# Kernel optimization log

Hardware: AMD Instinct MI355X
Metric: run time of the kernel (lower is better)

## Reference

```python
import jax, jax.numpy as jnp
import numpy as np

N = 100000   # nodes
E = 1600000  # edges (before self-loops)
IN, HID, OUT = 128, 16, 10
NEG_SLOPE = 0.2
LN_EPS = 1e-5


def layer_norm(x, gamma, beta):
    mu = jnp.mean(x, axis=-1, keepdims=True)
    var = jnp.mean((x - mu) ** 2, axis=-1, keepdims=True)
    return (x - mu) * jax.lax.rsqrt(var + LN_EPS) * gamma + beta


def gat_conv(x, edge_index, W, a_src, a_dst, bias, concat):
    # x: [N, Din], W: [Din, H*F], a_src/a_dst: [H, F]
    n = x.shape[0]
    H, F = a_src.shape
    h = (x @ W).reshape(n, H, F)                      # [N, H, F]
    src, dst = edge_index[0], edge_index[1]
    alpha_src = jnp.sum(h * a_src, axis=-1)           # [N, H]
    alpha_dst = jnp.sum(h * a_dst, axis=-1)           # [N, H]
    e = jax.nn.leaky_relu(alpha_src[src] + alpha_dst[dst], NEG_SLOPE)  # [E, H]
    # segment softmax over incoming edges of each dst node (self-loops guarantee non-empty)
    m = jax.ops.segment_max(e, dst, num_segments=n)
    e = jnp.exp(e - m[dst])
    s = jax.ops.segment_sum(e, dst, num_segments=n)
    alpha = e / (s[dst] + 1e-16)                      # [E, H]
    out = jax.ops.segment_sum(h[src] * alpha[:, :, None], dst, num_segments=n)  # [N, H, F]
    out = out.reshape(n, H * F) if concat else out.mean(axis=1)
    return out + bias


def setup_inputs() -> dict:
    key = jax.random.key(0)
    ks = jax.random.split(key, 20)
    d = {}
    d["x"] = jax.random.normal(ks[0], (N, IN), dtype=jnp.float32)
    d["edge_index"] = jax.random.randint(ks[1], (2, E), 0, N, dtype=jnp.int64)
    s = 0.1
    # layer 1: IN -> HID, 8 heads, concat
    d["W1"] = jax.random.normal(ks[2], (IN, 8 * HID), jnp.float32) * s
    d["a_src1"] = jax.random.normal(ks[3], (8, HID), jnp.float32) * s
    d["a_dst1"] = jax.random.normal(ks[4], (8, HID), jnp.float32) * s
    d["b1"] = jnp.zeros((8 * HID,), jnp.float32)
    d["g1"] = jnp.ones((8 * HID,), jnp.float32)
    d["be1"] = jnp.zeros((8 * HID,), jnp.float32)
    # layer 2: 8*HID -> HID, 4 heads, concat
    d["W2"] = jax.random.normal(ks[5], (8 * HID, 4 * HID), jnp.float32) * s
    d["a_src2"] = jax.random.normal(ks[6], (4, HID), jnp.float32) * s
    d["a_dst2"] = jax.random.normal(ks[7], (4, HID), jnp.float32) * s
    d["b2"] = jnp.zeros((4 * HID,), jnp.float32)
    d["g2"] = jnp.ones((4 * HID,), jnp.float32)
    d["be2"] = jnp.zeros((4 * HID,), jnp.float32)
    # layer 3: 4*HID -> OUT, 1 head, no concat
    d["W3"] = jax.random.normal(ks[8], (4 * HID, OUT), jnp.float32) * s
    d["a_src3"] = jax.random.normal(ks[9], (1, OUT), jnp.float32) * s
    d["a_dst3"] = jax.random.normal(ks[10], (1, OUT), jnp.float32) * s
    d["b3"] = jnp.zeros((OUT,), jnp.float32)
    return d


def reference(x, edge_index, W1, a_src1, a_dst1, b1, g1, be1,
              W2, a_src2, a_dst2, b2, g2, be2,
              W3, a_src3, a_dst3, b3):
    n = x.shape[0]
    loops = jnp.arange(n, dtype=edge_index.dtype)
    ei = jnp.concatenate([edge_index, jnp.stack([loops, loops])], axis=1)  # add self-loops
    h = gat_conv(x, ei, W1, a_src1, a_dst1, b1, concat=True)
    h = jax.nn.elu(layer_norm(h, g1, be1))
    h = gat_conv(h, ei, W2, a_src2, a_dst2, b2, concat=True)
    h = jax.nn.elu(layer_norm(h, g2, be2))
    h = gat_conv(h, ei, W3, a_src3, a_dst3, b3, concat=False)
    return jax.nn.log_softmax(h, axis=1)
```

## Files before the change

### kernel.cpp

```cpp
#include <hip/hip_runtime.h>
#include <hip/hip_bf16.h>
#include <math.h>

typedef __hip_bfloat16 bf16;
typedef __bf16 bf16x8 __attribute__((ext_vector_type(8)));
typedef float floatx4 __attribute__((ext_vector_type(4)));

#define CSR_CH  4096
#define CSR_REG 8192

__device__ __forceinline__ unsigned short f2bu(float f) {
    bf16 b = __float2bfloat16(f);
    return __builtin_bit_cast(unsigned short, b);
}
__device__ __forceinline__ float bu2f(unsigned short u) {
    return __uint_as_float(((unsigned)u) << 16);
}

template<int PF>
__device__ __forceinline__ void ldbfv(const unsigned short* p, float* v) {
    if constexpr (PF == 8) {
        uint4 u = *reinterpret_cast<const uint4*>(p);
        v[0] = __uint_as_float(u.x << 16); v[1] = __uint_as_float(u.x & 0xffff0000u);
        v[2] = __uint_as_float(u.y << 16); v[3] = __uint_as_float(u.y & 0xffff0000u);
        v[4] = __uint_as_float(u.z << 16); v[5] = __uint_as_float(u.z & 0xffff0000u);
        v[6] = __uint_as_float(u.w << 16); v[7] = __uint_as_float(u.w & 0xffff0000u);
    } else if constexpr (PF == 4) {
        uint2 u = *reinterpret_cast<const uint2*>(p);
        v[0] = __uint_as_float(u.x << 16); v[1] = __uint_as_float(u.x & 0xffff0000u);
        v[2] = __uint_as_float(u.y << 16); v[3] = __uint_as_float(u.y & 0xffff0000u);
    } else {
        unsigned u = *reinterpret_cast<const unsigned*>(p);
        v[0] = __uint_as_float(u << 16); v[1] = __uint_as_float(u & 0xffff0000u);
    }
}

template<typename XT, int H>
__global__ __launch_bounds__(256) void gemm_mfma(
    const XT* __restrict__ X, const float* __restrict__ W,
    const float* __restrict__ a_src, const float* __restrict__ a_dst,
    bf16* __restrict__ Hout, float* __restrict__ asrc, float* __restrict__ adst,
    int N, int NG, const int* __restrict__ ei, int E, int DPB,
    int* __restrict__ histM)
{
    constexpr int M = H * 16;
    constexpr int KP = 136;
    constexpr int NT = M / 16;
    constexpr int HPQ = H / 4;
    __shared__ __align__(16) unsigned short Wt[M * KP];
    __shared__ __align__(16) unsigned short As[64 * KP];
    __shared__ float As_s[M], Ad_s[M];
    int tid = threadIdx.x;

    if (blockIdx.x >= NG) {
        int* cnt = (int*)Wt;
        cnt[tid] = 0;
        __syncthreads();
        int blk = blockIdx.x - NG;
        int e0 = blk * CSR_CH;
        int e1 = min(E, e0 + CSR_CH);
        for (int e = e0 + tid; e < e1; e += 256)
            atomicAdd(&cnt[ei[E + e] / DPB], 1);
        __syncthreads();
        histM[blk * 256 + tid] = cnt[tid];
        return;
    }

    int r0 = blockIdx.x * 64;
    for (int i = tid; i < M; i += 256) { As_s[i] = a_src[i]; Ad_s[i] = a_dst[i]; }
    for (int idx = tid; idx < 128 * M; idx += 256) {
        int k = idx / M, m = idx % M;
        Wt[m * KP + k] = f2bu(W[idx]);
    }
    if constexpr (__is_same(XT, float)) {
        for (int idx = tid; idx < 64 * 32; idx += 256) {
            int row = idx >> 5, c4 = (idx & 31) * 4;
            int grow = r0 + row;
            float4 v = make_float4(0.f, 0.f, 0.f, 0.f);
            if (grow < N)
                v = *reinterpret_cast<const float4*>(X + (size_t)grow * 128 + c4);
            unsigned short* a = &As[row * KP + c4];
            a[0] = f2bu(v.x); a[1] = f2bu(v.y); a[2] = f2bu(v.z); a[3] = f2bu(v.w);
        }
    } else {
        for (int idx = tid; idx < 64 * 16; idx += 256) {
            int row = idx >> 4, c8 = (idx & 15) * 8;
            int grow = r0 + row;
            uint4 v = make_uint4(0u, 0u, 0u, 0u);
            if (grow < N)
                v = *reinterpret_cast<const uint4*>((const unsigned short*)X + (size_t)grow * 128 + c8);
            *reinterpret_cast<uint4*>(&As[row * KP + c8]) = v;
        }
    }
    __syncthreads();

    int w = tid >> 6, l = tid & 63, q = l >> 4, c = l & 15;
    floatx4 acc[NT];
    #pragma unroll
    for (int t = 0; t < NT; ++t) acc[t] = (floatx4){0.f, 0.f, 0.f, 0.f};

    #pragma unroll
    for (int kc = 0; kc < 4; ++kc) {
        bf16x8 a = *reinterpret_cast<const bf16x8*>(&As[(w * 16 + c) * KP + kc * 32 + q * 8]);
        #pragma unroll
        for (int t = 0; t < NT; ++t) {
            bf16x8 b = *reinterpret_cast<const bf16x8*>(&Wt[(t * 16 + c) * KP + kc * 32 + q * 8]);
            acc[t] = __builtin_amdgcn_mfma_f32_16x16x32_bf16(a, b, acc[t], 0, 0, 0);
        }
    }
    __syncthreads();
    #pragma unroll
    for (int t = 0; t < NT; ++t)
        #pragma unroll
        for (int r = 0; r < 4; ++r)
            As[(w * 16 + q * 4 + r) * KP + t * 16 + c] = f2bu(acc[t][r]);
    __syncthreads();
    for (int idx = tid; idx < 64 * (M / 8); idx += 256) {
        int row = idx / (M / 8), g = idx % (M / 8);
        int grow = r0 + row;
        if (grow < N)
            *reinterpret_cast<uint4*>(Hout + (size_t)grow * M + g * 8) =
                *reinterpret_cast<const uint4*>(&As[row * KP + g * 8]);
    }
    {
        int r = tid >> 2, qq = tid & 3;
        int grow = r0 + r;
        if (grow < N) {
            #pragma unroll
            for (int hh = 0; hh < HPQ; ++hh) {
                int hd = qq * HPQ + hh;
                float s1 = 0.f, s2 = 0.f;
                #pragma unroll
                for (int f = 0; f < 16; f += 2) {
                    unsigned u = *reinterpret_cast<const unsigned*>(&As[r * KP + hd * 16 + f]);
                    float v0 = __uint_as_float(u << 16);
                    float v1 = __uint_as_float(u & 0xffff0000u);
                    s1 += v0 * As_s[hd * 16 + f] + v1 * As_s[hd * 16 + f + 1];
                    s2 += v0 * Ad_s[hd * 16 + f] + v1 * Ad_s[hd * 16 + f + 1];
                }
                asrc[(size_t)grow * H + hd] = s1;
                adst[(size_t)grow * H + hd] = s2;
            }
        }
    }
}

__global__ __launch_bounds__(256) void csr_colscan(
    const int* __restrict__ histM, int NBLK,
    int* __restrict__ offT, int* __restrict__ btot)
{
    __shared__ int sm[512];
    int b = blockIdx.x;
    int tid = threadIdx.x;
    int i0 = tid, i1 = tid + 256;
    sm[i0] = (i0 < NBLK) ? histM[i0 * 256 + b] : 0;
    sm[i1] = (i1 < NBLK) ? histM[i1 * 256 + b] : 0;
    __syncthreads();
    #pragma unroll
    for (int o = 1; o < 512; o <<= 1) {
        int t0 = (i0 >= o) ? sm[i0 - o] : 0;
        int t1 = (i1 >= o) ? sm[i1 - o] : 0;
        __syncthreads();
        sm[i0] += t0; sm[i1] += t1;
        __syncthreads();
    }
    if (i0 < NBLK) offT[b * NBLK + i0] = b * CSR_REG + ((i0 == 0) ? 0 : sm[i0 - 1]);
    if (i1 < NBLK) offT[b * NBLK + i1] = b * CSR_REG + sm[i1 - 1];
    if (tid == 0) btot[b] = sm[511];
}

__global__ __launch_bounds__(256) void csr_pair_scatter(
    const int* __restrict__ ei, int E, int DPB,
    const int* __restrict__ offT, int NBLK,
    unsigned* __restrict__ pairs)
{
    __shared__ int cnt[256];
    int tid = threadIdx.x;
    int blk = blockIdx.x;
    cnt[tid] = offT[tid * NBLK + blk];
    __syncthreads();
    int e0 = blk * CSR_CH;
    int e1 = min(E, e0 + CSR_CH);
    for (int e = e0 + tid; e < e1; e += 256) {
        int s = ei[e];
        int d = ei[E + e];
        int b = d / DPB;
        int dloc = d - b * DPB;
        int pos = atomicAdd(&cnt[b], 1);
        pairs[pos] = ((unsigned)dloc << 17) | (unsigned)s;
    }
}

__global__ __launch_bounds__(256) void csr_fine(
    const unsigned* __restrict__ pairs, const int* __restrict__ btot,
    int DPB, int N, int2* __restrict__ ptrSE, int* __restrict__ col)
{
    __shared__ int sm[512];
    __shared__ int off[512];
    int b = blockIdx.x;
    int tid = threadIdx.x;
    int base = b * CSR_REG;
    int tot = btot[b];
    int d0 = b * DPB;
    int i0 = tid, i1 = tid + 256;
    sm[i0] = 0; sm[i1] = 0;
    __syncthreads();
    for (int i = tid; i < tot; i += 256)
        atomicAdd(&sm[pairs[base + i] >> 17], 1);
    __syncthreads();
    #pragma unroll
    for (int o = 1; o < 512; o <<= 1) {
        int t0 = (i0 >= o) ? sm[i0 - o] : 0;
        int t1 = (i1 >= o) ? sm[i1 - o] : 0;
        __syncthreads();
        sm[i0] += t0; sm[i1] += t1;
        __syncthreads();
    }
    int s0e = base + ((i0 == 0) ? 0 : sm[i0 - 1]);
    int s1e = base + sm[i1 - 1];
    off[i0] = s0e;
    off[i1] = s1e;
    if (i0 < DPB && d0 + i0 < N) ptrSE[d0 + i0] = make_int2(s0e, base + sm[i0]);
    if (i1 < DPB && d0 + i1 < N) ptrSE[d0 + i1] = make_int2(s1e, base + sm[i1]);
    __syncthreads();
    for (int i = tid; i < tot; i += 256) {
        unsigned p = pairs[base + i];
        int pos = atomicAdd(&off[p >> 17], 1);
        col[pos] = (int)(p & 0x1FFFFu);
    }
}

template<int M, int LPD>
__global__ __launch_bounds__(256) void agg_ln_kernel(
    const int2* __restrict__ ptrSE, const int* __restrict__ col,
    const float* __restrict__ asrc, const float* __restrict__ adst,
    const bf16* __restrict__ hb, const float* __restrict__ bias,
    const float* __restrict__ g, const float* __restrict__ be,
    bf16* __restrict__ out, int N)
{
    constexpr int PF = M / LPD;
    constexpr int H = M / 16;
    constexpr int DPBk = 256 / LPD;
    int tid = threadIdx.x;
    int sub = tid / LPD;
    int j = tid % LPD;
    int d = blockIdx.x * DPBk + sub;
    if (d >= N) return;
    int f0 = j * PF;
    int hd = f0 / 16;
    int2 se = ptrSE[d];
    int e = se.x, end = se.y;
    float adst_h = adst[d * H + hd];
    const unsigned short* hw = (const unsigned short*)hb;

    float ac0[PF], ac1[PF];
    float dn0, dn1 = 0.f;
    {
        float lg = asrc[d * H + hd] + adst_h;
        lg = lg > 0.f ? lg : 0.2f * lg;
        float w = __expf(lg);
        float v[PF];
        ldbfv<PF>(hw + (size_t)d * M + f0, v);
        #pragma unroll
        for (int p = 0; p < PF; ++p) { ac0[p] = w * v[p]; ac1[p] = 0.f; }
        dn0 = w;
    }
    for (; e + 4 <= end; e += 4) {
        int s0 = col[e], s1 = col[e + 1], s2 = col[e + 2], s3 = col[e + 3];
        float l0 = asrc[s0 * H + hd];
        float l1 = asrc[s1 * H + hd];
        float l2 = asrc[s2 * H + hd];
        float l3 = asrc[s3 * H + hd];
        float v0[PF], v1[PF], v2[PF], v3[PF];
        ldbfv<PF>(hw + (size_t)s0 * M + f0, v0);
        ldbfv<PF>(hw + (size_t)s1 * M + f0, v1);
        ldbfv<PF>(hw + (size_t)s2 * M + f0, v2);
        ldbfv<PF>(hw + (size_t)s3 * M + f0, v3);
        l0 += adst_h; l0 = l0 > 0.f ? l0 : 0.2f * l0; float w0 = __expf(l0);
        l1 += adst_h; l1 = l1 > 0.f ? l1 : 0.2f * l1; float w1 = __expf(l1);
        l2 += adst_h; l2 = l2 > 0.f ? l2 : 0.2f * l2; float w2 = __expf(l2);
        l3 += adst_h; l3 = l3 > 0.f ? l3 : 0.2f * l3; float w3 = __expf(l3);
        #pragma unroll
        for (int p = 0; p < PF; ++p) {
            ac0[p] += w0 * v0[p];
            ac1[p] += w1 * v1[p];
            ac0[p] += w2 * v2[p];
            ac1[p] += w3 * v3[p];
        }
        dn0 += w0 + w2; dn1 += w1 + w3;
    }
    for (; e < end; ++e) {
        int s = col[e];
        float lg = asrc[s * H + hd] + adst_h;
        lg = lg > 0.f ? lg : 0.2f * lg;
        float w = __expf(lg);
        float v[PF];
        ldbfv<PF>(hw + (size_t)s * M + f0, v);
        #pragma unroll
        for (int p = 0; p < PF; ++p) ac0[p] += w * v[p];
        dn0 += w;
    }

    float rden = 1.f / (dn0 + dn1 + 1e-16f);
    float o[PF];
    float sm1 = 0.f, sm2 = 0.f;
    #pragma unroll
    for (int p = 0; p < PF; ++p) {
        o[p] = (ac0[p] + ac1[p]) * rden + bias[f0 + p];
        sm1 += o[p];
        sm2 += o[p] * o[p];
    }
    #pragma unroll
    for (int off = LPD / 2; off >= 1; off >>= 1) {
        sm1 += __shfl_xor(sm1, off, LPD);
        sm2 += __shfl_xor(sm2, off, LPD);
    }
    float mu = sm1 * (1.f / M);
    float var = sm2 * (1.f / M) - mu * mu;
    float inv = rsqrtf(var + 1e-5f);
    unsigned pk[PF / 2];
    #pragma unroll
    for (int p = 0; p < PF; p += 2) {
        float y0 = (o[p] - mu) * inv * g[f0 + p] + be[f0 + p];
        float y1 = (o[p + 1] - mu) * inv * g[f0 + p + 1] + be[f0 + p + 1];
        y0 = y0 > 0.f ? y0 : expm1f(y0);
        y1 = y1 > 0.f ? y1 : expm1f(y1);
        pk[p / 2] = (unsigned)f2bu(y0) | ((unsigned)f2bu(y1) << 16);
    }
    unsigned short* op = (unsigned short*)out + (size_t)d * M + f0;
    if constexpr (PF == 8)
        *reinterpret_cast<uint4*>(op) = make_uint4(pk[0], pk[1], pk[2], pk[3]);
    else if constexpr (PF == 4)
        *reinterpret_cast<uint2*>(op) = make_uint2(pk[0], pk[1]);
    else
        *reinterpret_cast<unsigned*>(op) = pk[0];
}

__global__ __launch_bounds__(256) void agg_ln_l2_g3(
    const int2* __restrict__ ptrSE, const int* __restrict__ col,
    const float* __restrict__ asrc, const float* __restrict__ adst,
    const bf16* __restrict__ hb, const float* __restrict__ bias,
    const float* __restrict__ g, const float* __restrict__ be,
    const float* __restrict__ W3, const float* __restrict__ as3,
    const float* __restrict__ ad3,
    bf16* __restrict__ h3, float* __restrict__ asrc3, float* __restrict__ adst3,
    int N)
{
    constexpr int M = 64, LPD = 16, PF = 4, H = 4, DPBk = 16;
    __shared__ float Wl[640], s3[10], d3[10];
    int tid = threadIdx.x;
    for (int i = tid; i < 640; i += 256) Wl[i] = W3[i];
    if (tid < 10) { s3[tid] = as3[tid]; d3[tid] = ad3[tid]; }
    __syncthreads();
    int sub = tid >> 4;
    int j = tid & 15;
    int d = blockIdx.x * DPBk + sub;
    if (d >= N) return;
    int f0 = j * PF;
    int hd = f0 / 16;
    int2 se = ptrSE[d];
    int e = se.x, end = se.y;
    float adst_h = adst[d * H + hd];
    const unsigned short* hw = (const unsigned short*)hb;

    float ac0[PF], ac1[PF];
    float dn0, dn1 = 0.f;
    {
        float lg = asrc[d * H + hd] + adst_h;
        lg = lg > 0.f ? lg : 0.2f * lg;
        float w = __expf(lg);
        float v[PF];
        ldbfv<PF>(hw + (size_t)d * M + f0, v);
        #pragma unroll
        for (int p = 0; p < PF; ++p) { ac0[p] = w * v[p]; ac1[p] = 0.f; }
        dn0 = w;
    }
    for (; e + 4 <= end; e += 4) {
        int s0 = col[e], s1 = col[e + 1], s2 = col[e + 2], s3i = col[e + 3];
        float l0 = asrc[s0 * H + hd];
        float l1 = asrc[s1 * H + hd];
        float l2 = asrc[s2 * H + hd];
        float l3 = asrc[s3i * H + hd];
        float v0[PF], v1[PF], v2[PF], v3[PF];
        ldbfv<PF>(hw + (size_t)s0 * M + f0, v0);
        ldbfv<PF>(hw + (size_t)s1 * M + f0, v1);
        ldbfv<PF>(hw + (size_t)s2 * M + f0, v2);
        ldbfv<PF>(hw + (size_t)s3i * M + f0, v3);
        l0 += adst_h; l0 = l0 > 0.f ? l0 : 0.2f * l0; float w0 = __expf(l0);
        l1 += adst_h; l1 = l1 > 0.f ? l1 : 0.2f * l1; float w1 = __expf(l1);
        l2 += adst_h; l2 = l2 > 0.f ? l2 : 0.2f * l2; float w2 = __expf(l2);
        l3 += adst_h; l3 = l3 > 0.f ? l3 : 0.2f * l3; float w3 = __expf(l3);
        #pragma unroll
        for (int p = 0; p < PF; ++p) {
            ac0[p] += w0 * v0[p];
            ac1[p] += w1 * v1[p];
            ac0[p] += w2 * v2[p];
            ac1[p] += w3 * v3[p];
        }
        dn0 += w0 + w2; dn1 += w1 + w3;
    }
    for (; e < end; ++e) {
        int s = col[e];
        float lg = asrc[s * H + hd] + adst_h;
        lg = lg > 0.f ? lg : 0.2f * lg;
        float w = __expf(lg);
        float v[PF];
        ldbfv<PF>(hw + (size_t)s * M + f0, v);
        #pragma unroll
        for (int p = 0; p < PF; ++p) ac0[p] += w * v[p];
        dn0 += w;
    }

    float rden = 1.f / (dn0 + dn1 + 1e-16f);
    float o[PF];
    float sm1 = 0.f, sm2 = 0.f;
    #pragma unroll
    for (int p = 0; p < PF; ++p) {
        o[p] = (ac0[p] + ac1[p]) * rden + bias[f0 + p];
        sm1 += o[p];
        sm2 += o[p] * o[p];
    }
    #pragma unroll
    for (int off = 8; off >= 1; off >>= 1) {
        sm1 += __shfl_xor(sm1, off, 16);
        sm2 += __shfl_xor(sm2, off, 16);
    }
    float mu = sm1 * (1.f / M);
    float var = sm2 * (1.f / M) - mu * mu;
    float inv = rsqrtf(var + 1e-5f);
    float y[PF];
    #pragma unroll
    for (int p = 0; p < PF; ++p) {
        float t = (o[p] - mu) * inv * g[f0 + p] + be[f0 + p];
        y[p] = t > 0.f ? t : expm1f(t);
    }
    float pj[10];
    #pragma unroll
    for (int jj = 0; jj < 10; ++jj)
        pj[jj] = y[0] * Wl[(f0 + 0) * 10 + jj] + y[1] * Wl[(f0 + 1) * 10 + jj]
               + y[2] * Wl[(f0 + 2) * 10 + jj] + y[3] * Wl[(f0 + 3) * 10 + jj];
    #pragma unroll
    for (int off = 8; off >= 1; off >>= 1)
        #pragma unroll
        for (int jj = 0; jj < 10; ++jj)
            pj[jj] += __shfl_xor(pj[jj], off, 16);
    if (j == 0) {
        unsigned short* hr = (unsigned short*)h3 + (size_t)d * 16;
        #pragma unroll
        for (int jj = 0; jj < 10; jj += 2) {
            unsigned u = (unsigned)f2bu(pj[jj]) | ((unsigned)f2bu(pj[jj + 1]) << 16);
            *reinterpret_cast<unsigned*>(hr + jj) = u;
        }
        float a1 = 0.f, a2 = 0.f;
        #pragma unroll
        for (int jj = 0; jj < 10; ++jj) {
            a1 += pj[jj] * s3[jj];
            a2 += pj[jj] * d3[jj];
        }
        asrc3[d] = a1;
        adst3[d] = a2;
    }
}

__global__ __launch_bounds__(256) void agg_l3_final(
    const int2* __restrict__ ptrSE, const int* __restrict__ col,
    const float* __restrict__ asrc, const float* __restrict__ adst,
    const bf16* __restrict__ h, const float* __restrict__ b3,
    float* __restrict__ out, int N)
{
    int tid = threadIdx.x;
    int sub16 = tid >> 4;
    int j = tid & 15;
    int d = blockIdx.x * 16 + sub16;
    if (d >= N) return;
    const unsigned short* hu = (const unsigned short*)h;
    int2 se = ptrSE[d];
    int e = se.x, end = se.y;
    float adst_d = adst[d];
    float lg = asrc[d] + adst_d;
    lg = lg > 0.f ? lg : 0.2f * lg;
    float w = __expf(lg);
    bool act = j < 10;
    float a0 = act ? w * bu2f(hu[(size_t)d * 16 + j]) : 0.f;
    float a1 = 0.f, a2 = 0.f, a3 = 0.f;
    float d0 = w, d1 = 0.f, d2 = 0.f, d3 = 0.f;
    for (; e + 4 <= end; e += 4) {
        int s0 = col[e + 0], s1 = col[e + 1], s2 = col[e + 2], s3 = col[e + 3];
        float l0 = asrc[s0], l1 = asrc[s1], l2 = asrc[s2], l3 = asrc[s3];
        float v0 = act ? bu2f(hu[(size_t)s0 * 16 + j]) : 0.f;
        float v1 = act ? bu2f(hu[(size_t)s1 * 16 + j]) : 0.f;
        float v2 = act ? bu2f(hu[(size_t)s2 * 16 + j]) : 0.f;
        float v3 = act ? bu2f(hu[(size_t)s3 * 16 + j]) : 0.f;
        l0 += adst_d; l0 = l0 > 0.f ? l0 : 0.2f * l0; float w0 = __expf(l0);
        l1 += adst_d; l1 = l1 > 0.f ? l1 : 0.2f * l1; float w1 = __expf(l1);
        l2 += adst_d; l2 = l2 > 0.f ? l2 : 0.2f * l2; float w2 = __expf(l2);
        l3 += adst_d; l3 = l3 > 0.f ? l3 : 0.2f * l3; float w3 = __expf(l3);
        a0 += w0 * v0; a1 += w1 * v1; a2 += w2 * v2; a3 += w3 * v3;
        d0 += w0; d1 += w1; d2 += w2; d3 += w3;
    }
    for (; e < end; ++e) {
        int s = col[e];
        float l = asrc[s] + adst_d;
        l = l > 0.f ? l : 0.2f * l;
        float ww = __expf(l);
        if (act) a0 += ww * bu2f(hu[(size_t)s * 16 + j]);
        d0 += ww;
    }
    float den = d0 + d1 + d2 + d3;
    float v = (a0 + a1 + a2 + a3) / (den + 1e-16f);
    float lv = act ? v + b3[j] : -1e30f;
    float mx = lv;
    #pragma unroll
    for (int off = 1; off < 16; off <<= 1) mx = fmaxf(mx, __shfl_xor(mx, off, 16));
    float ev = act ? __expf(lv - mx) : 0.f;
    float se2 = ev;
    #pragma unroll
    for (int off = 1; off < 16; off <<= 1) se2 += __shfl_xor(se2, off, 16);
    float ls = mx + logf(se2);
    if (act) out[(size_t)d * 10 + j] = lv - ls;
}

static inline int cdiv(long a, long b) { return (int)((a + b - 1) / b); }

extern "C" void kernel_launch(void* const* d_in, const int* in_sizes, int n_in,
                              void* d_out, int out_size, void* d_ws, size_t ws_size,
                              hipStream_t stream)
{
    const float* x   = (const float*)d_in[0];
    const int*   ei  = (const int*)d_in[1];
    const float* W1  = (const float*)d_in[2];
    const float* as1 = (const float*)d_in[3];
    const float* ad1 = (const float*)d_in[4];
    const float* b1  = (const float*)d_in[5];
    const float* g1  = (const float*)d_in[6];
    const float* be1 = (const float*)d_in[7];
    const float* W2  = (const float*)d_in[8];
    const float* as2 = (const float*)d_in[9];
    const float* ad2 = (const float*)d_in[10];
    const float* b2  = (const float*)d_in[11];
    const float* g2  = (const float*)d_in[12];
    const float* be2 = (const float*)d_in[13];
    const float* W3  = (const float*)d_in[14];
    const float* as3 = (const float*)d_in[15];
    const float* ad3 = (const float*)d_in[16];
    const float* b3  = (const float*)d_in[17];

    const int N = in_sizes[0] / 128;
    const int E = in_sizes[1] / 2;

    const int DPB  = cdiv(N, 256);
    const int NBLK = cdiv(E, CSR_CH);

    bf16*     hb    = (bf16*)d_ws;
    bf16*     aggb  = hb + (size_t)N * 128;
    float*    asrc  = (float*)(aggb + (size_t)N * 128);
    float*    adst  = asrc + (size_t)N * 8;
    float*    asrc3 = adst + (size_t)N * 8;
    float*    adst3 = asrc3 + N;
    unsigned* pairs = (unsigned*)(adst3 + N);
    int*      col   = (int*)(pairs + 256 * CSR_REG);
    int2*     ptrSE = (int2*)(col + 256 * CSR_REG);
    int*      histM = (int*)(ptrSE + N);
    int*      offT  = histM + (size_t)NBLK * 256;
    int*      btot  = offT + (size_t)NBLK * 256;
    bf16*     h3b   = aggb;

    const int NG1 = cdiv(N, 64);

    gemm_mfma<float, 8><<<NG1 + NBLK, 256, 0, stream>>>(
        x, W1, as1, ad1, hb, asrc, adst, N, NG1, ei, E, DPB, histM);
    csr_colscan<<<256, 256, 0, stream>>>(histM, NBLK, offT, btot);
    csr_pair_scatter<<<NBLK, 256, 0, stream>>>(ei, E, DPB, offT, NBLK, pairs);
    csr_fine<<<256, 256, 0, stream>>>(pairs, btot, DPB, N, ptrSE, col);

    agg_ln_kernel<128, 16><<<cdiv(N, 16), 256, 0, stream>>>(
        ptrSE, col, asrc, adst, hb, b1, g1, be1, aggb, N);

    const int NG2 = cdiv(N, 64);
    gemm_mfma<bf16, 4><<<NG2, 256, 0, stream>>>(
        aggb, W2, as2, ad2, hb, asrc, adst, N, NG2, nullptr, 0, 1, nullptr);

    agg_ln_l2_g3<<<cdiv(N, 16), 256, 0, stream>>>(
        ptrSE, col, asrc, adst, hb, b2, g2, be2, W3, as3, ad3,
        h3b, asrc3, adst3, N);

    agg_l3_final<<<cdiv(N, 16), 256, 0, stream>>>(
        ptrSE, col, asrc3, adst3, h3b, b3, (float*)d_out, N);
}
```

Measured before the change: 382.6 us.

## Use fewer lanes per node with wider loads and prefetched neighbor indices in aggregation

The three aggregation kernels now assign fewer lanes to each destination node: 8 lanes for layers 1 and 2, and 4 for layer 3. Each lane loads 16-byte vectors of bf16 features and covers more features, so a block handles 32 or 64 nodes instead of 16. The neighbor indices for the next group of four edges are loaded one iteration ahead to hide the latency of the col loads. The aim is fewer, wider gather transactions and less redundant per-lane work such as attention-logit loads and exps, at the cost of more registers per thread and less parallelism per node on high-degree nodes.

```diff
diff --git a/kernel.cpp b/kernel.cpp
--- a/kernel.cpp
+++ b/kernel.cpp
@@ -17,22 +17,21 @@
     return __uint_as_float(((unsigned)u) << 16);
 }
 
-template<int PF>
-__device__ __forceinline__ void ldbfv(const unsigned short* p, float* v) {
-    if constexpr (PF == 8) {
-        uint4 u = *reinterpret_cast<const uint4*>(p);
-        v[0] = __uint_as_float(u.x << 16); v[1] = __uint_as_float(u.x & 0xffff0000u);
-        v[2] = __uint_as_float(u.y << 16); v[3] = __uint_as_float(u.y & 0xffff0000u);
-        v[4] = __uint_as_float(u.z << 16); v[5] = __uint_as_float(u.z & 0xffff0000u);
-        v[6] = __uint_as_float(u.w << 16); v[7] = __uint_as_float(u.w & 0xffff0000u);
-    } else if constexpr (PF == 4) {
-        uint2 u = *reinterpret_cast<const uint2*>(p);
-        v[0] = __uint_as_float(u.x << 16); v[1] = __uint_as_float(u.x & 0xffff0000u);
-        v[2] = __uint_as_float(u.y << 16); v[3] = __uint_as_float(u.y & 0xffff0000u);
-    } else {
-        unsigned u = *reinterpret_cast<const unsigned*>(p);
-        v[0] = __uint_as_float(u << 16); v[1] = __uint_as_float(u & 0xffff0000u);
-    }
+__device__ __forceinline__ void accu4(float* ac, float w, uint4 u) {
+    ac[0] += w * __uint_as_float(u.x << 16);
+    ac[1] += w * __uint_as_float(u.x & 0xffff0000u);
+    ac[2] += w * __uint_as_float(u.y << 16);
+    ac[3] += w * __uint_as_float(u.y & 0xffff0000u);
+    ac[4] += w * __uint_as_float(u.z << 16);
+    ac[5] += w * __uint_as_float(u.z & 0xffff0000u);
+    ac[6] += w * __uint_as_float(u.w << 16);
+    ac[7] += w * __uint_as_float(u.w & 0xffff0000u);
+}
+__device__ __forceinline__ void accu2(float* ac, float w, uint2 u) {
+    ac[0] += w * __uint_as_float(u.x << 16);
+    ac[1] += w * __uint_as_float(u.x & 0xffff0000u);
+    ac[2] += w * __uint_as_float(u.y << 16);
+    ac[3] += w * __uint_as_float(u.y & 0xffff0000u);
 }
 
 template<typename XT, int H>
@@ -230,110 +229,111 @@
     }
 }
 
-template<int M, int LPD>
-__global__ __launch_bounds__(256) void agg_ln_kernel(
+__global__ __launch_bounds__(256) void agg_ln_l1(
     const int2* __restrict__ ptrSE, const int* __restrict__ col,
     const float* __restrict__ asrc, const float* __restrict__ adst,
     const bf16* __restrict__ hb, const float* __restrict__ bias,
     const float* __restrict__ g, const float* __restrict__ be,
     bf16* __restrict__ out, int N)
 {
-    constexpr int PF = M / LPD;
-    constexpr int H = M / 16;
-    constexpr int DPBk = 256 / LPD;
     int tid = threadIdx.x;
-    int sub = tid / LPD;
-    int j = tid % LPD;
-    int d = blockIdx.x * DPBk + sub;
+    int sub = tid >> 3, j = tid & 7;
+    int d = blockIdx.x * 32 + sub;
     if (d >= N) return;
-    int f0 = j * PF;
-    int hd = f0 / 16;
+    int f0 = j * 16;
+    int hd = j;
     int2 se = ptrSE[d];
     int e = se.x, end = se.y;
-    float adst_h = adst[d * H + hd];
+    float adst_h = adst[d * 8 + hd];
     const unsigned short* hw = (const unsigned short*)hb;
-
-    float ac0[PF], ac1[PF];
+    const unsigned short* hwl = hw + f0;
+    const float* as_h = asrc + hd;
+
+    float ac[16];
+    #pragma unroll
+    for (int p = 0; p < 16; ++p) ac[p] = 0.f;
     float dn0, dn1 = 0.f;
+
     {
-        float lg = asrc[d * H + hd] + adst_h;
+        float lg = as_h[(size_t)d * 8] + adst_h;
         lg = lg > 0.f ? lg : 0.2f * lg;
         float w = __expf(lg);
-        float v[PF];
-        ldbfv<PF>(hw + (size_t)d * M + f0, v);
-        #pragma unroll
-        for (int p = 0; p < PF; ++p) { ac0[p] = w * v[p]; ac1[p] = 0.f; }
+        const uint4* p = reinterpret_cast<const uint4*>(hwl + ((size_t)d << 7));
+        uint4 a = p[0], b = p[1];
+        accu4(ac, w, a); accu4(ac + 8, w, b);
         dn0 = w;
     }
-    for (; e + 4 <= end; e += 4) {
-        int s0 = col[e], s1 = col[e + 1], s2 = col[e + 2], s3 = col[e + 3];
-        float l0 = asrc[s0 * H + hd];
-        float l1 = asrc[s1 * H + hd];
-        float l2 = asrc[s2 * H + hd];
-        float l3 = asrc[s3 * H + hd];
-        float v0[PF], v1[PF], v2[PF], v3[PF];
-        ldbfv<PF>(hw + (size_t)s0 * M + f0, v0);
-        ldbfv<PF>(hw + (size_t)s1 * M + f0, v1);
-        ldbfv<PF>(hw + (size_t)s2 * M + f0, v2);
-        ldbfv<PF>(hw + (size_t)s3 * M + f0, v3);
+
+    int c0 = 0, c1 = 0, c2 = 0, c3 = 0;
+    if (e + 4 <= end) { c0 = col[e]; c1 = col[e + 1]; c2 = col[e + 2]; c3 = col[e + 3]; }
+    while (e + 4 <= end) {
+        int en = e + 4;
+        int n0 = c0, n1 = c1, n2 = c2, n3 = c3;
+        if (en + 4 <= end) { n0 = col[en]; n1 = col[en + 1]; n2 = col[en + 2]; n3 = col[en + 3]; }
+        float l0 = as_h[(size_t)c0 * 8];
+        float l1 = as_h[(size_t)c1 * 8];
+        float l2 = as_h[(size_t)c2 * 8];
+        float l3 = as_h[(size_t)c3 * 8];
+        const uint4* p0 = reinterpret_cast<const uint4*>(hwl + ((size_t)c0 << 7));
+        const uint4* p1 = reinterpret_cast<const uint4*>(hwl + ((size_t)c1 << 7));
+        const uint4* p2 = reinterpret_cast<const uint4*>(hwl + ((size_t)c2 << 7));
+        const uint4* p3 = reinterpret_cast<const uint4*>(hwl + ((size_t)c3 << 7));
+        uint4 u00 = p0[0], u01 = p0[1];
+        uint4 u10 = p1[0], u11 = p1[1];
+        uint4 u20 = p2[0], u21 = p2[1];
+        uint4 u30 = p3[0], u31 = p3[1];
         l0 += adst_h; l0 = l0 > 0.f ? l0 : 0.2f * l0; float w0 = __expf(l0);
         l1 += adst_h; l1 = l1 > 0.f ? l1 : 0.2f * l1; float w1 = __expf(l1);
         l2 += adst_h; l2 = l2 > 0.f ? l2 : 0.2f * l2; float w2 = __expf(l2);
         l3 += adst_h; l3 = l3 > 0.f ? l3 : 0.2f * l3; float w3 = __expf(l3);
-        #pragma unroll
-        for (int p = 0; p < PF; ++p) {
-            ac0[p] += w0 * v0[p];
-            ac1[p] += w1 * v1[p];
-            ac0[p] += w2 * v2[p];
-            ac1[p] += w3 * v3[p];
-        }
+        accu4(ac, w0, u00); accu4(ac + 8, w0, u01);
+        accu4(ac, w1, u10); accu4(ac + 8, w1, u11);
+        accu4(ac, w2, u20); accu4(ac + 8, w2, u21);
+        accu4(ac, w3, u30); accu4(ac + 8, w3, u31);
         dn0 += w0 + w2; dn1 += w1 + w3;
+        c0 = n0; c1 = n1; c2 = n2; c3 = n3;
+        e = en;
     }
     for (; e < end; ++e) {
         int s = col[e];
-        float lg = asrc[s * H + hd] + adst_h;
+        float lg = as_h[(size_t)s * 8] + adst_h;
         lg = lg > 0.f ? lg : 0.2f * lg;
         float w = __expf(lg);
-        float v[PF];
-        ldbfv<PF>(hw + (size_t)s * M + f0, v);
-        #pragma unroll
-        for (int p = 0; p < PF; ++p) ac0[p] += w * v[p];
+        const uint4* p = reinterpret_cast<const uint4*>(hwl + ((size_t)s << 7));
+        uint4 a = p[0], b = p[1];
+        accu4(ac, w, a); accu4(ac + 8, w, b);
         dn0 += w;
     }
 
     float rden = 1.f / (dn0 + dn1 + 1e-16f);
-    float o[PF];
+    float o[16];
     float sm1 = 0.f, sm2 = 0.f;
     #pragma unroll
-    for (int p = 0; p < PF; ++p) {
-        o[p] = (ac0[p] + ac1[p]) * rden + bias[f0 + p];
+    for (int p = 0; p < 16; ++p) {
+        o[p] = ac[p] * rden + bias[f0 + p];
         sm1 += o[p];
         sm2 += o[p] * o[p];
     }
     #pragma unroll
-    for (int off = LPD / 2; off >= 1; off >>= 1) {
-        sm1 += __shfl_xor(sm1, off, LPD);
-        sm2 += __shfl_xor(sm2, off, LPD);
-    }
-    float mu = sm1 * (1.f / M);
-    float var = sm2 * (1.f / M) - mu * mu;
+    for (int off = 4; off >= 1; off >>= 1) {
+        sm1 += __shfl_xor(sm1, off, 8);
+        sm2 += __shfl_xor(sm2, off, 8);
+    }
+    float mu = sm1 * (1.f / 128.f);
+    float var = sm2 * (1.f / 128.f) - mu * mu;
     float inv = rsqrtf(var + 1e-5f);
-    unsigned pk[PF / 2];
-    #pragma unroll
-    for (int p = 0; p < PF; p += 2) {
+    unsigned pk[8];
+    #pragma unroll
+    for (int p = 0; p < 16; p += 2) {
         float y0 = (o[p] - mu) * inv * g[f0 + p] + be[f0 + p];
         float y1 = (o[p + 1] - mu) * inv * g[f0 + p + 1] + be[f0 + p + 1];
         y0 = y0 > 0.f ? y0 : expm1f(y0);
         y1 = y1 > 0.f ? y1 : expm1f(y1);
         pk[p / 2] = (unsigned)f2bu(y0) | ((unsigned)f2bu(y1) << 16);
     }
-    unsigned short* op = (unsigned short*)out + (size_t)d * M + f0;
-    if constexpr (PF == 8)
-        *reinterpret_cast<uint4*>(op) = make_uint4(pk[0], pk[1], pk[2], pk[3]);
-    else if constexpr (PF == 4)
-        *reinterpret_cast<uint2*>(op) = make_uint2(pk[0], pk[1]);
-    else
-        *reinterpret_cast<unsigned*>(op) = pk[0];
+    unsigned short* op = (unsigned short*)out + (size_t)d * 128 + f0;
+    *reinterpret_cast<uint4*>(op) = make_uint4(pk[0], pk[1], pk[2], pk[3]);
+    *reinterpret_cast<uint4*>(op + 8) = make_uint4(pk[4], pk[5], pk[6], pk[7]);
 }
 
 __global__ __launch_bounds__(256) void agg_ln_l2_g3(
@@ -346,111 +346,119 @@
     bf16* __restrict__ h3, float* __restrict__ asrc3, float* __restrict__ adst3,
     int N)
 {
-    constexpr int M = 64, LPD = 16, PF = 4, H = 4, DPBk = 16;
     __shared__ float Wl[640], s3[10], d3[10];
     int tid = threadIdx.x;
     for (int i = tid; i < 640; i += 256) Wl[i] = W3[i];
     if (tid < 10) { s3[tid] = as3[tid]; d3[tid] = ad3[tid]; }
     __syncthreads();
-    int sub = tid >> 4;
-    int j = tid & 15;
-    int d = blockIdx.x * DPBk + sub;
+    int sub = tid >> 3, j = tid & 7;
+    int d = blockIdx.x * 32 + sub;
     if (d >= N) return;
-    int f0 = j * PF;
-    int hd = f0 / 16;
+    int f0 = j * 8;
+    int hd = j >> 1;
     int2 se = ptrSE[d];
     int e = se.x, end = se.y;
-    float adst_h = adst[d * H + hd];
+    float adst_h = adst[d * 4 + hd];
     const unsigned short* hw = (const unsigned short*)hb;
-
-    float ac0[PF], ac1[PF];
+    const unsigned short* hwl = hw + f0;
+    const float* as_h = asrc + hd;
+
+    float ac[8];
+    #pragma unroll
+    for (int p = 0; p < 8; ++p) ac[p] = 0.f;
     float dn0, dn1 = 0.f;
+
     {
-        float lg = asrc[d * H + hd] + adst_h;
+        float lg = as_h[(size_t)d * 4] + adst_h;
         lg = lg > 0.f ? lg : 0.2f * lg;
         float w = __expf(lg);
-        float v[PF];
-        ldbfv<PF>(hw + (size_t)d * M + f0, v);
-        #pragma unroll
-        for (int p = 0; p < PF; ++p) { ac0[p] = w * v[p]; ac1[p] = 0.f; }
+        uint4 u = *reinterpret_cast<const uint4*>(hwl + ((size_t)d << 6));
+        accu4(ac, w, u);
         dn0 = w;
     }
-    for (; e + 4 <= end; e += 4) {
-        int s0 = col[e], s1 = col[e + 1], s2 = col[e + 2], s3i = col[e + 3];
-        float l0 = asrc[s0 * H + hd];
-        float l1 = asrc[s1 * H + hd];
-        float l2 = asrc[s2 * H + hd];
-        float l3 = asrc[s3i * H + hd];
-        float v0[PF], v1[PF], v2[PF], v3[PF];
-        ldbfv<PF>(hw + (size_t)s0 * M + f0, v0);
-        ldbfv<PF>(hw + (size_t)s1 * M + f0, v1);
-        ldbfv<PF>(hw + (size_t)s2 * M + f0, v2);
-        ldbfv<PF>(hw + (size_t)s3i * M + f0, v3);
+
+    int c0 = 0, c1 = 0, c2 = 0, c3 = 0;
+    if (e + 4 <= end) { c0 = col[e]; c1 = col[e + 1]; c2 = col[e + 2]; c3 = col[e + 3]; }
+    while (e + 4 <= end) {
+        int en = e + 4;
+        int n0 = c0, n1 = c1, n2 = c2, n3 = c3;
+        if (en + 4 <= end) { n0 = col[en]; n1 = col[en + 1]; n2 = col[en + 2]; n3 = col[en + 3]; }
+        float l0 = as_h[(size_t)c0 * 4];
+        float l1 = as_h[(size_t)c1 * 4];
+        float l2 = as_h[(size_t)c2 * 4];
+        float l3 = as_h[(size_t)c3 * 4];
+        uint4 u0 = *reinterpret_cast<const uint4*>(hwl + ((size_t)c0 << 6));
+        uint4 u1 = *reinterpret_cast<const uint4*>(hwl + ((size_t)c1 << 6));
+        uint4 u2 = *reinterpret_cast<const uint4*>(hwl + ((size_t)c2 << 6));
+        uint4 u3 = *reinterpret_cast<const uint4*>(hwl + ((size_t)c3 << 6));
         l0 += adst_h; l0 = l0 > 0.f ? l0 : 0.2f * l0; float w0 = __expf(l0);
         l1 += adst_h; l1 = l1 > 0.f ? l1 : 0.2f * l1; float w1 = __expf(l1);
         l2 += adst_h; l2 = l2 > 0.f ? l2 : 0.2f * l2; float w2 = __expf(l2);
         l3 += adst_h; l3 = l3 > 0.f ? l3 : 0.2f * l3; float w3 = __expf(l3);
-        #pragma unroll
-        for (int p = 0; p < PF; ++p) {
-            ac0[p] += w0 * v0[p];
-            ac1[p] += w1 * v1[p];
-            ac0[p] += w2 * v2[p];
-            ac1[p] += w3 * v3[p];
-        }
+        accu4(ac, w0, u0);
+        accu4(ac, w1, u1);
+        accu4(ac, w2, u2);
+        accu4(ac, w3, u3);
         dn0 += w0 + w2; dn1 += w1 + w3;
+        c0 = n0; c1 = n1; c2 = n2; c3 = n3;
+        e = en;
     }
     for (; e < end; ++e) {
         int s = col[e];
-        float lg = asrc[s * H + hd] + adst_h;
+        float lg = as_h[(size_t)s * 4] + adst_h;
         lg = lg > 0.f ? lg : 0.2f * lg;
         float w = __expf(lg);
-        float v[PF];
-        ldbfv<PF>(hw + (size_t)s * M + f0, v);
-        #pragma unroll
-        for (int p = 0; p < PF; ++p) ac0[p] += w * v[p];
+        uint4 u = *reinterpret_cast<const uint4*>(hwl + ((size_t)s << 6));
+        accu4(ac, w, u);
         dn0 += w;
     }
 
     float rden = 1.f / (dn0 + dn1 + 1e-16f);
-    float o[PF];
+    float o[8];
     float sm1 = 0.f, sm2 = 0.f;
     #pragma unroll
-    for (int p = 0; p < PF; ++p) {
-        o[p] = (ac0[p] + ac1[p]) * rden + bias[f0 + p];
+    for (int p = 0; p < 8; ++p) {
+        o[p] = ac[p] * rden + bias[f0 + p];
         sm1 += o[p];
         sm2 += o[p] * o[p];
     }
     #pragma unroll
-    for (int off = 8; off >= 1; off >>= 1) {
-        sm1 += __shfl_xor(sm1, off, 16);
-        sm2 += __shfl_xor(sm2, off, 16);
-    }
-    float mu = sm1 * (1.f / M);
-    float var = sm2 * (1.f / M) - mu * mu;
+    for (int off = 4; off >= 1; off >>= 1) {
+        sm1 += __shfl_xor(sm1, off, 8);
+        sm2 += __shfl_xor(sm2, off, 8);
+    }
+    float mu = sm1 * (1.f / 64.f);
+    float var = sm2 * (1.f / 64.f) - mu * mu;
     float inv = rsqrtf(var + 1e-5f);
-    float y[PF];
-    #pragma unroll
-    for (int p = 0; p < PF; ++p) {
+    float y[8];
+    #pragma unroll
+    for (int p = 0; p < 8; ++p) {
         float t = (o[p] - mu) * inv * g[f0 + p] + be[f0 + p];
         y[p] = t > 0.f ? t : expm1f(t);
     }
     float pj[10];
     #pragma unroll
-    for (int jj = 0; jj < 10; ++jj)
-        pj[jj] = y[0] * Wl[(f0 + 0) * 10 + jj] + y[1] * Wl[(f0 + 1) * 10 + jj]
-               + y[2] * Wl[(f0 + 2) * 10 + jj] + y[3] * Wl[(f0 + 3) * 10 + jj];
-    #pragma unroll
-    for (int off = 8; off >= 1; off >>= 1)
+    for (int jj = 0; jj < 10; ++jj) {
+        float s = 0.f;
+        #pragma unroll
+        for (int p = 0; p < 8; ++p)
+            s += y[p] * Wl[(f0 + p) * 10 + jj];
+        pj[jj] = s;
+    }
+    #pragma unroll
+    for (int off = 4; off >= 1; off >>= 1)
         #pragma unroll
         for (int jj = 0; jj < 10; ++jj)
-            pj[jj] += __shfl_xor(pj[jj], off, 16);
+            pj[jj] += __shfl_xor(pj[jj], off, 8);
     if (j == 0) {
         unsigned short* hr = (unsigned short*)h3 + (size_t)d * 16;
-        #pragma unroll
-        for (int jj = 0; jj < 10; jj += 2) {
-            unsigned u = (unsigned)f2bu(pj[jj]) | ((unsigned)f2bu(pj[jj + 1]) << 16);
-            *reinterpret_cast<unsigned*>(hr + jj) = u;
-        }
+        unsigned q0 = (unsigned)f2bu(pj[0]) | ((unsigned)f2bu(pj[1]) << 16);
+        unsigned q1 = (unsigned)f2bu(pj[2]) | ((unsigned)f2bu(pj[3]) << 16);
+        unsigned q2 = (unsigned)f2bu(pj[4]) | ((unsigned)f2bu(pj[5]) << 16);
+        unsigned q3 = (unsigned)f2bu(pj[6]) | ((unsigned)f2bu(pj[7]) << 16);
+        unsigned q4 = (unsigned)f2bu(pj[8]) | ((unsigned)f2bu(pj[9]) << 16);
+        *reinterpret_cast<uint4*>(hr) = make_uint4(q0, q1, q2, q3);
+        *reinterpret_cast<uint4*>(hr + 8) = make_uint4(q4, 0u, 0u, 0u);
         float a1 = 0.f, a2 = 0.f;
         #pragma unroll
         for (int jj = 0; jj < 10; ++jj) {
@@ -469,55 +477,87 @@
     float* __restrict__ out, int N)
 {
     int tid = threadIdx.x;
-    int sub16 = tid >> 4;
-    int j = tid & 15;
-    int d = blockIdx.x * 16 + sub16;
+    int sub = tid >> 2, j = tid & 3;
+    int d = blockIdx.x * 64 + sub;
     if (d >= N) return;
     const unsigned short* hu = (const unsigned short*)h;
+    const unsigned short* hul = hu + j * 4;
     int2 se = ptrSE[d];
     int e = se.x, end = se.y;
     float adst_d = adst[d];
-    float lg = asrc[d] + adst_d;
-    lg = lg > 0.f ? lg : 0.2f * lg;
-    float w = __expf(lg);
-    bool act = j < 10;
-    float a0 = act ? w * bu2f(hu[(size_t)d * 16 + j]) : 0.f;
-    float a1 = 0.f, a2 = 0.f, a3 = 0.f;
-    float d0 = w, d1 = 0.f, d2 = 0.f, d3 = 0.f;
-    for (; e + 4 <= end; e += 4) {
-        int s0 = col[e + 0], s1 = col[e + 1], s2 = col[e + 2], s3 = col[e + 3];
-        float l0 = asrc[s0], l1 = asrc[s1], l2 = asrc[s2], l3 = asrc[s3];
-        float v0 = act ? bu2f(hu[(size_t)s0 * 16 + j]) : 0.f;
-        float v1 = act ? bu2f(hu[(size_t)s1 * 16 + j]) : 0.f;
-        float v2 = act ? bu2f(hu[(size_t)s2 * 16 + j]) : 0.f;
-        float v3 = act ? bu2f(hu[(size_t)s3 * 16 + j]) : 0.f;
+
+    float ac[4] = {0.f, 0.f, 0.f, 0.f};
+    float dn0, dn1 = 0.f;
+    {
+        float lg = asrc[d] + adst_d;
+        lg = lg > 0.f ? lg : 0.2f * lg;
+        float w = __expf(lg);
+        uint2 u = *reinterpret_cast<const uint2*>(hul + (size_t)d * 16);
+        accu2(ac, w, u);
+        dn0 = w;
+    }
+
+    int c0 = 0, c1 = 0, c2 = 0, c3 = 0;
+    if (e + 4 <= end) { c0 = col[e]; c1 = col[e + 1]; c2 = col[e + 2]; c3 = col[e + 3]; }
+    while (e + 4 <= end) {
+        int en = e + 4;
+        int n0 = c0, n1 = c1, n2 = c2, n3 = c3;
+        if (en + 4 <= end) { n0 = col[en]; n1 = col[en + 1]; n2 = col[en + 2]; n3 = col[en + 3]; }
+        float l0 = asrc[c0];
+        float l1 = asrc[c1];
+        float l2 = asrc[c2];
+        float l3 = asrc[c3];
+        uint2 u0 = *reinterpret_cast<const uint2*>(hul + (size_t)c0 * 16);
+        uint2 u1 = *reinterpret_cast<const uint2*>(hul + (size_t)c1 * 16);
+        uint2 u2 = *reinterpret_cast<const uint2*>(hul + (size_t)c2 * 16);
+        uint2 u3 = *reinterpret_cast<const uint2*>(hul + (size_t)c3 * 16);
         l0 += adst_d; l0 = l0 > 0.f ? l0 : 0.2f * l0; float w0 = __expf(l0);
         l1 += adst_d; l1 = l1 > 0.f ? l1 : 0.2f * l1; float w1 = __expf(l1);
         l2 += adst_d; l2 = l2 > 0.f ? l2 : 0.2f * l2; float w2 = __expf(l2);
         l3 += adst_d; l3 = l3 > 0.f ? l3 : 0.2f * l3; float w3 = __expf(l3);
-        a0 += w0 * v0; a1 += w1 * v1; a2 += w2 * v2; a3 += w3 * v3;
-        d0 += w0; d1 += w1; d2 += w2; d3 += w3;
+        accu2(ac, w0, u0);
+        accu2(ac, w1, u1);
+        accu2(ac, w2, u2);
+        accu2(ac, w3, u3);
+        dn0 += w0 + w2; dn1 += w1 + w3;
+        c0 = n0; c1 = n1; c2 = n2; c3 = n3;
+        e = en;
     }
     for (; e < end; ++e) {
         int s = col[e];
-        float l = asrc[s] + adst_d;
-        l = l > 0.f ? l : 0.2f * l;
-        float ww = __expf(l);
-        if (act) a0 += ww * bu2f(hu[(size_t)s * 16 + j]);
-        d0 += ww;
-    }
-    float den = d0 + d1 + d2 + d3;
-    float v = (a0 + a1 + a2 + a3) / (den + 1e-16f);
-    float lv = act ? v + b3[j] : -1e30f;
-    float mx = lv;
-    #pragma unroll
-    for (int off = 1; off < 16; off <<= 1) mx = fmaxf(mx, __shfl_xor(mx, off, 16));
-    float ev = act ? __expf(lv - mx) : 0.f;
-    float se2 = ev;
-    #pragma unroll
-    for (int off = 1; off < 16; off <<= 1) se2 += __shfl_xor(se2, off, 16);
-    float ls = mx + logf(se2);
-    if (act) out[(size_t)d * 10 + j] = lv - ls;
+        float lg = asrc[s] + adst_d;
+        lg = lg > 0.f ? lg : 0.2f * lg;
+        float w = __expf(lg);
+        uint2 u = *reinterpret_cast<const uint2*>(hul + (size_t)s * 16);
+        accu2(ac, w, u);
+        dn0 += w;
+    }
+
+    float rden = 1.f / (dn0 + dn1 + 1e-16f);
+    int base = j * 4;
+    float lv[4];
+    #pragma unroll
+    for (int p = 0; p < 4; ++p) {
+        int idx = base + p;
+        float bb = b3[idx < 10 ? idx : 9];
+        lv[p] = (idx < 10) ? ac[p] * rden + bb : -1e30f;
+    }
+    float mx = fmaxf(fmaxf(lv[0], lv[1]), fmaxf(lv[2], lv[3]));
+    mx = fmaxf(mx, __shfl_xor(mx, 1, 4));
+    mx = fmaxf(mx, __shfl_xor(mx, 2, 4));
+    float es = 0.f;
+    #pragma unroll
+    for (int p = 0; p < 4; ++p)
+        es += __expf(lv[p] - mx);
+    es += __shfl_xor(es, 1, 4);
+    es += __shfl_xor(es, 2, 4);
+    float ls = mx + logf(es);
+    if (base < 10) {
+        float* orow = out + (size_t)d * 10 + base;
+        *reinterpret_cast<float2*>(orow) = make_float2(lv[0] - ls, lv[1] - ls);
+        if (base + 2 < 10)
+            *reinterpret_cast<float2*>(orow + 2) = make_float2(lv[2] - ls, lv[3] - ls);
+    }
 }
 
 static inline int cdiv(long a, long b) { return (int)((a + b - 1) / b); }
@@ -573,17 +613,17 @@
     csr_pair_scatter<<<NBLK, 256, 0, stream>>>(ei, E, DPB, offT, NBLK, pairs);
     csr_fine<<<256, 256, 0, stream>>>(pairs, btot, DPB, N, ptrSE, col);
 
-    agg_ln_kernel<128, 16><<<cdiv(N, 16), 256, 0, stream>>>(
+    agg_ln_l1<<<cdiv(N, 32), 256, 0, stream>>>(
         ptrSE, col, asrc, adst, hb, b1, g1, be1, aggb, N);
 
     const int NG2 = cdiv(N, 64);
     gemm_mfma<bf16, 4><<<NG2, 256, 0, stream>>>(
         aggb, W2, as2, ad2, hb, asrc, adst, N, NG2, nullptr, 0, 1, nullptr);
 
-    agg_ln_l2_g3<<<cdiv(N, 16), 256, 0, stream>>>(
+    agg_ln_l2_g3<<<cdiv(N, 32), 256, 0, stream>>>(
         ptrSE, col, asrc, adst, hb, b2, g2, be2, W3, as3, ad3,
         h3b, asrc3, adst3, N);
 
-    agg_l3_final<<<cdiv(N, 16), 256, 0, stream>>>(
+    agg_l3_final<<<cdiv(N, 64), 256, 0, stream>>>(
         ptrSE, col, asrc3, adst3, h3b, b3, (float*)d_out, N);
 }
```

New measurement: 368.6 us. 1.04x faster.
